# Optimization experiments

Measured on AMD Instinct MI355X. Metric: run time of the kernel, lower is better.

## Reference

```python
import jax, jax.numpy as jnp
import numpy as np

H, W, C_IN, C_OUT, B = 256, 256, 64, 64, 2
NEG_SLOPE = 0.2


def make_grid_edges(h, w, b):
    """8-neighborhood grid edges + self-loops (GATConv add_self_loops), batched with node offsets."""
    idx = np.arange(h * w).reshape(h, w)
    src_l, dst_l = [], []
    for dr in (-1, 0, 1):
        for dc in (-1, 0, 1):
            rs = slice(max(0, -dr), h - max(0, dr))
            cs = slice(max(0, -dc), w - max(0, dc))
            dst = idx[rs, cs]
            src = idx[rs.start + dr:rs.stop + dr, cs.start + dc:cs.stop + dc]
            src_l.append(src.ravel())
            dst_l.append(dst.ravel())
    s = np.concatenate(src_l)
    d = np.concatenate(dst_l)
    offs = (np.arange(b) * h * w)[:, None]
    return (s[None] + offs).ravel().astype(np.int32), (d[None] + offs).ravel().astype(np.int32)


def setup_inputs() -> dict:
    key = jax.random.key(0)
    ks = jax.random.split(key, 7)
    x = jax.random.normal(ks[0], (B, C_IN, H, W), dtype=jnp.float32)
    pos_w = jax.random.normal(ks[1], (2, C_IN), dtype=jnp.float32) * (1.0 / np.sqrt(2.0))
    pos_b = jax.random.normal(ks[2], (C_IN,), dtype=jnp.float32) * 0.1
    lin_w = jax.random.normal(ks[3], (C_IN, C_OUT), dtype=jnp.float32) * (1.0 / np.sqrt(C_IN))
    att_src = jax.random.normal(ks[4], (C_OUT,), dtype=jnp.float32) * (1.0 / np.sqrt(C_OUT))
    att_dst = jax.random.normal(ks[5], (C_OUT,), dtype=jnp.float32) * (1.0 / np.sqrt(C_OUT))
    bias = jax.random.normal(ks[6], (C_OUT,), dtype=jnp.float32) * 0.1
    es, ed = make_grid_edges(H, W, B)
    return {"x": x, "pos_w": pos_w, "pos_b": pos_b, "lin_w": lin_w,
            "att_src": att_src, "att_dst": att_dst, "bias": bias,
            "edge_src": jnp.asarray(es), "edge_dst": jnp.asarray(ed)}


def reference(x, pos_w, pos_b, lin_w, att_src, att_dst, bias, edge_src, edge_dst):
    b, c, h, w = x.shape
    n = h * w
    num_nodes = b * n
    # positional encoding: pos[h,w] = (y, x) in [-1,1]
    px = jnp.linspace(-1.0, 1.0, w)
    py = jnp.linspace(-1.0, 1.0, h)
    gx, gy = jnp.meshgrid(px, py, indexing="xy")          # (H, W)
    pos = jnp.stack([gy, gx], axis=-1)                     # (H, W, 2)
    pe = pos @ pos_w + pos_b                               # (H, W, C)
    xg = (x + pe.transpose(2, 0, 1)[None]).transpose(0, 2, 3, 1).reshape(num_nodes, c)
    # GATConv, heads=1: linear transform, per-edge attention logits
    hfeat = xg @ lin_w                                     # (BN, Cout)
    a_src = hfeat @ att_src                                # (BN,)
    a_dst = hfeat @ att_dst                                # (BN,)
    e = jax.nn.leaky_relu(a_src[edge_src] + a_dst[edge_dst], NEG_SLOPE)  # (E,)
    # segment softmax over incoming edges of each target node
    m = jax.ops.segment_max(e, edge_dst, num_segments=num_nodes)
    p = jnp.exp(e - m[edge_dst])
    s = jax.ops.segment_sum(p, edge_dst, num_segments=num_nodes)
    alpha = p / s[edge_dst]                                # (E,)
    # scatter-add aggregation of weighted messages
    out = jax.ops.segment_sum(alpha[:, None] * hfeat[edge_src], edge_dst,
                              num_segments=num_nodes) + bias
    return out.reshape(b, h, w, -1).transpose(0, 3, 1, 2)
```

## Files before the change

### kernel.cpp

```cpp
#include <hip/hip_runtime.h>

#define HGT 256
#define WID 256
#define CH  64
#define NB  2
#define HW  (HGT * WID)
#define NODES (NB * HW)
#define NEG_SLOPE 0.2f


__device__ __forceinline__ unsigned short f2bf(float f) {
    union { float f; unsigned u; } v; v.f = f;
    unsigned r = v.u + 0x7FFF + ((v.u >> 16) & 1);
    return (unsigned short)(r >> 16);
}

__global__ __launch_bounds__(256) void gat_feat(
    const float* __restrict__ x, const float* __restrict__ pos_w,
    const float* __restrict__ pos_b, const float* __restrict__ lin_w,
    const float* __restrict__ att_src, const float* __restrict__ att_dst,
    unsigned short* __restrict__ hfeat, float* __restrict__ asrc,
    float* __restrict__ adst)
{
    __shared__ float xs[CH][64];
    __shared__ float W0[CH], W1[CH], Bc[CH];
    __shared__ float red_s[4][64], red_d[4][64];

    const int tid = threadIdx.x;
    const int tx  = tid & 63;
    const int ty  = tid >> 6;

    const int raw = blockIdx.x;
    const int wg  = (raw & 7) * 256 + (raw >> 3);
    const int chunk = wg & 3;
    const int bi    = wg >> 2;
    const int i     = bi & (HGT - 1);
    const int b     = bi >> 8;
    const int j     = chunk * 64 + tx;
    const int hw    = i * WID + j;

    const float* xb = x + (size_t)b * CH * HW + hw;
    #pragma unroll
    for (int r = 0; r < 16; ++r) {
        const int ci = ty * 16 + r;
        xs[ci][tx] = xb[(size_t)ci * HW];
    }

    if (tid < CH) {
        float w0 = 0.f, w1 = 0.f, bc = 0.f;
        for (int ci = 0; ci < CH; ++ci) {
            float lwv = lin_w[ci * CH + tid];
            w0 = fmaf(pos_w[ci],      lwv, w0);
            w1 = fmaf(pos_w[CH + ci], lwv, w1);
            bc = fmaf(pos_b[ci],      lwv, bc);
        }
        W0[tid] = w0; W1[tid] = w1; Bc[tid] = bc;
    }
    __syncthreads();

    const int cob = __builtin_amdgcn_readfirstlane(ty) * 16;

    float acc[16];
    #pragma unroll
    for (int k = 0; k < 16; ++k) acc[k] = 0.f;

    const float* lw = lin_w + cob;
    #pragma unroll
    for (int ci = 0; ci < CH; ++ci) {
        const float xv = xs[ci][tx];
        #pragma unroll
        for (int k = 0; k < 16; ++k)
            acc[k] = fmaf(xv, lw[ci * CH + k], acc[k]);
    }

    const float py  = -1.f + (2.f / 255.f) * (float)i;
    const float pxv = -1.f + (2.f / 255.f) * (float)j;

    float as = 0.f, ad = 0.f;
    unsigned pk[8];
    #pragma unroll
    for (int k = 0; k < 16; ++k) {
        const int co = cob + k;
        const float h = acc[k] + py * W0[co] + pxv * W1[co] + Bc[co];
        as = fmaf(h, att_src[co], as);
        ad = fmaf(h, att_dst[co], ad);
        const unsigned short bf = f2bf(h);
        if (k & 1) pk[k >> 1] |= (unsigned)bf << 16;
        else       pk[k >> 1]  = bf;
    }
    uint2* hq = (uint2*)hfeat + (size_t)(b * 16 + (cob >> 2)) * HW + hw;
    #pragma unroll
    for (int qq = 0; qq < 4; ++qq)
        hq[(size_t)qq * HW] = make_uint2(pk[2 * qq], pk[2 * qq + 1]);

    red_s[ty][tx] = as; red_d[ty][tx] = ad;
    __syncthreads();
    if (ty == 0) {
        const int node = b * HW + hw;
        asrc[node] = red_s[0][tx] + red_s[1][tx] + red_s[2][tx] + red_s[3][tx];
        adst[node] = red_d[0][tx] + red_d[1][tx] + red_d[2][tx] + red_d[3][tx];
    }
}

__global__ __launch_bounds__(256) void gat_aggr(
    const unsigned short* __restrict__ hfeat, const float* __restrict__ asrc,
    const float* __restrict__ adst, const float* __restrict__ bias,
    float* __restrict__ out)
{
    const int tid = threadIdx.x;
    const int tx  = tid & 63;
    const int ty  = tid >> 6;

    const int raw = blockIdx.x;
    const int wg  = (raw & 7) * 1024 + (raw >> 3);
    const int qg    = wg & 3;
    const int chunk = (wg >> 2) & 3;
    const int bi    = wg >> 4;
    const int i     = bi & (HGT - 1);
    const int b     = bi >> 8;
    const int j     = chunk * 64 + tx;
    const int hw    = i * WID + j;
    const int node  = b * HW + hw;
    const int q     = __builtin_amdgcn_readfirstlane(qg * 4 + ty);

    const float adv = adst[node];

    float w[9];
    int   off[9];
    float m = -1e30f;
    #pragma unroll
    for (int t = 0; t < 9; ++t) {
        const int dr = t / 3 - 1, dc = t % 3 - 1;
        const int r = i + dr, c = j + dc;
        const bool ok = (r >= 0) && (r < HGT) && (c >= 0) && (c < WID);
        off[t] = ok ? (dr * WID + dc) : 0;
        float ev = -1e30f;
        if (ok) {
            ev = asrc[node + off[t]] + adv;
            ev = (ev >= 0.f) ? ev : NEG_SLOPE * ev;
        }
        w[t] = ev;
        m = fmaxf(m, ev);
    }

    float s = 0.f;
    #pragma unroll
    for (int t = 0; t < 9; ++t) {
        const float p = (w[t] > -1e29f) ? __expf(w[t] - m) : 0.f;
        w[t] = p; s += p;
    }
    const float inv = 1.f / s;

    const uint2* hq = (const uint2*)hfeat + (size_t)(b * 16 + q) * HW + hw;

    float a0 = 0.f, a1 = 0.f, a2 = 0.f, a3 = 0.f;
    #pragma unroll
    for (int t = 0; t < 9; ++t) {
        const uint2 v  = hq[off[t]];
        const float wt = w[t] * inv;
        a0 = fmaf(wt, __uint_as_float(v.x << 16),         a0);
        a1 = fmaf(wt, __uint_as_float(v.x & 0xffff0000u), a1);
        a2 = fmaf(wt, __uint_as_float(v.y << 16),         a2);
        a3 = fmaf(wt, __uint_as_float(v.y & 0xffff0000u), a3);
    }

    float* ob = out + (size_t)(b * CH + q * 4) * HW + hw;
    ob[0 * (size_t)HW] = a0 + bias[q * 4 + 0];
    ob[1 * (size_t)HW] = a1 + bias[q * 4 + 1];
    ob[2 * (size_t)HW] = a2 + bias[q * 4 + 2];
    ob[3 * (size_t)HW] = a3 + bias[q * 4 + 3];
}

extern "C" void kernel_launch(void* const* d_in, const int* in_sizes, int n_in,
                              void* d_out, int out_size, void* d_ws, size_t ws_size,
                              hipStream_t stream) {
    const float* x       = (const float*)d_in[0];
    const float* pos_w   = (const float*)d_in[1];
    const float* pos_b   = (const float*)d_in[2];
    const float* lin_w   = (const float*)d_in[3];
    const float* att_src = (const float*)d_in[4];
    const float* att_dst = (const float*)d_in[5];
    const float* bias    = (const float*)d_in[6];

    float* out = (float*)d_out;
    unsigned short* hfeat = (unsigned short*)d_ws;
    float* asrc = (float*)((char*)d_ws + (size_t)NODES * CH * 2);
    float* adst = asrc + NODES;

    gat_feat<<<dim3(2048), dim3(256), 0, stream>>>(
        x, pos_w, pos_b, lin_w, att_src, att_dst, hfeat, asrc, adst);
    gat_aggr<<<dim3(8192), dim3(256), 0, stream>>>(
        hfeat, asrc, adst, bias, out);
}
```

Before: 150.2 us.

## Compute node feature projection with bf16 MFMA instead of scalar FMA

Rewrites the feature-projection kernel so each wavefront handles 32 nodes and runs the 64x64 linear transform as bf16 32x32x16 MFMA instructions. The lin_w weights are converted to bf16 and stored swizzled in LDS, and x is cast to bf16 in registers. This replaces the scalar FMA loop and its LDS staging of x. It also changes the launch to 512 blocks of 512 threads and reduces the attention dot products with a lane shuffle. The cost is lower precision, since both the inputs and the weights are now rounded to bf16 before the matmul.

```diff
diff --git a/kernel.cpp b/kernel.cpp
--- a/kernel.cpp
+++ b/kernel.cpp
@@ -8,6 +8,8 @@
 #define NODES (NB * HW)
 #define NEG_SLOPE 0.2f
 
+typedef float f32x16 __attribute__((ext_vector_type(16)));
+typedef short short8 __attribute__((ext_vector_type(8)));
 
 __device__ __forceinline__ unsigned short f2bf(float f) {
     union { float f; unsigned u; } v; v.f = f;
@@ -15,91 +17,127 @@
     return (unsigned short)(r >> 16);
 }
 
-__global__ __launch_bounds__(256) void gat_feat(
+__global__ __launch_bounds__(512) void gat_feat(
     const float* __restrict__ x, const float* __restrict__ pos_w,
     const float* __restrict__ pos_b, const float* __restrict__ lin_w,
     const float* __restrict__ att_src, const float* __restrict__ att_dst,
     unsigned short* __restrict__ hfeat, float* __restrict__ asrc,
     float* __restrict__ adst)
 {
-    __shared__ float xs[CH][64];
-    __shared__ float W0[CH], W1[CH], Bc[CH];
-    __shared__ float red_s[4][64], red_d[4][64];
-
-    const int tid = threadIdx.x;
-    const int tx  = tid & 63;
-    const int ty  = tid >> 6;
-
-    const int raw = blockIdx.x;
-    const int wg  = (raw & 7) * 256 + (raw >> 3);
-    const int chunk = wg & 3;
-    const int bi    = wg >> 2;
-    const int i     = bi & (HGT - 1);
-    const int b     = bi >> 8;
-    const int j     = chunk * 64 + tx;
-    const int hw    = i * WID + j;
-
-    const float* xb = x + (size_t)b * CH * HW + hw;
-    #pragma unroll
-    for (int r = 0; r < 16; ++r) {
-        const int ci = ty * 16 + r;
-        xs[ci][tx] = xb[(size_t)ci * HW];
-    }
-
+    __shared__ __align__(16) unsigned char wlds[CH * 128];
+    __shared__ __align__(16) float W0s[CH], W1s[CH], Bcs[CH], atts[CH], attd[CH];
+
+    const int tid  = threadIdx.x;
+    const int lane = tid & 63;
+    const int wid  = tid >> 6;
+    const int hi   = lane >> 5;
+    const int col  = lane & 31;
+
+    {
+        const int co  = tid & 63;
+        const int cib = (tid >> 6) * 8;
+        unsigned char* rowp = wlds + co * 128;
+        const unsigned sw = (unsigned)((co & 7) << 4);
+        #pragma unroll
+        for (int p = 0; p < 4; ++p) {
+            const int ci = cib + 2 * p;
+            const unsigned lo = f2bf(lin_w[ci * CH + co]);
+            const unsigned hh = f2bf(lin_w[(ci + 1) * CH + co]);
+            *(unsigned*)(rowp + (((unsigned)(2 * ci)) ^ sw)) = lo | (hh << 16);
+        }
+    }
     if (tid < CH) {
         float w0 = 0.f, w1 = 0.f, bc = 0.f;
         for (int ci = 0; ci < CH; ++ci) {
-            float lwv = lin_w[ci * CH + tid];
+            const float lwv = lin_w[ci * CH + tid];
             w0 = fmaf(pos_w[ci],      lwv, w0);
             w1 = fmaf(pos_w[CH + ci], lwv, w1);
             bc = fmaf(pos_b[ci],      lwv, bc);
         }
-        W0[tid] = w0; W1[tid] = w1; Bc[tid] = bc;
+        W0s[tid] = w0; W1s[tid] = w1; Bcs[tid] = bc;
+    } else if (tid < 128) {
+        atts[tid - 64] = att_src[tid - 64];
+    } else if (tid < 192) {
+        attd[tid - 128] = att_dst[tid - 128];
     }
     __syncthreads();
 
-    const int cob = __builtin_amdgcn_readfirstlane(ty) * 16;
-
-    float acc[16];
-    #pragma unroll
-    for (int k = 0; k < 16; ++k) acc[k] = 0.f;
-
-    const float* lw = lin_w + cob;
-    #pragma unroll
-    for (int ci = 0; ci < CH; ++ci) {
-        const float xv = xs[ci][tx];
-        #pragma unroll
-        for (int k = 0; k < 16; ++k)
-            acc[k] = fmaf(xv, lw[ci * CH + k], acc[k]);
-    }
-
-    const float py  = -1.f + (2.f / 255.f) * (float)i;
-    const float pxv = -1.f + (2.f / 255.f) * (float)j;
-
+    short8 a0[4], a1[4];
+    {
+        const unsigned sw = (unsigned)((col & 7) << 4);
+        #pragma unroll
+        for (int ks = 0; ks < 4; ++ks) {
+            const unsigned off = (unsigned)(32 * ks + 16 * hi) ^ sw;
+            a0[ks] = *(const short8*)(wlds + col * 128 + off);
+            a1[ks] = *(const short8*)(wlds + (32 + col) * 128 + off);
+        }
+    }
+
+    const int g     = blockIdx.x * 8 + wid;
+    const int node0 = g * 32;
+    const int b     = node0 >> 16;
+    const int hw    = (node0 & (HW - 1)) + col;
+    const int node  = node0 + col;
+
+    const float* xp = x + (size_t)b * CH * HW + hw;
+    float xv[32];
+    #pragma unroll
+    for (int ks = 0; ks < 4; ++ks)
+        #pragma unroll
+        for (int e = 0; e < 8; ++e)
+            xv[ks * 8 + e] = xp[(size_t)(16 * ks + 8 * hi + e) * HW];
+
+    short8 bk[4];
+    #pragma unroll
+    for (int ks = 0; ks < 4; ++ks)
+        #pragma unroll
+        for (int e = 0; e < 8; ++e)
+            bk[ks][e] = (short)f2bf(xv[ks * 8 + e]);
+
+    f32x16 acc0, acc1;
+    #pragma unroll
+    for (int k = 0; k < 16; ++k) { acc0[k] = 0.f; acc1[k] = 0.f; }
+
+    #pragma unroll
+    for (int ks = 0; ks < 4; ++ks) {
+        acc0 = __builtin_amdgcn_mfma_f32_32x32x16_bf16(a0[ks], bk[ks], acc0, 0, 0, 0);
+        acc1 = __builtin_amdgcn_mfma_f32_32x32x16_bf16(a1[ks], bk[ks], acc1, 0, 0, 0);
+    }
+
+    const int ii = hw >> 8, jj = hw & 255;
+    const float py = -1.f + (2.f / 255.f) * (float)ii;
+    const float px = -1.f + (2.f / 255.f) * (float)jj;
+
+    uint2* hq = (uint2*)hfeat + (size_t)b * 16 * HW + hw;
     float as = 0.f, ad = 0.f;
-    unsigned pk[8];
-    #pragma unroll
-    for (int k = 0; k < 16; ++k) {
-        const int co = cob + k;
-        const float h = acc[k] + py * W0[co] + pxv * W1[co] + Bc[co];
-        as = fmaf(h, att_src[co], as);
-        ad = fmaf(h, att_dst[co], ad);
-        const unsigned short bf = f2bf(h);
-        if (k & 1) pk[k >> 1] |= (unsigned)bf << 16;
-        else       pk[k >> 1]  = bf;
-    }
-    uint2* hq = (uint2*)hfeat + (size_t)(b * 16 + (cob >> 2)) * HW + hw;
-    #pragma unroll
-    for (int qq = 0; qq < 4; ++qq)
-        hq[(size_t)qq * HW] = make_uint2(pk[2 * qq], pk[2 * qq + 1]);
-
-    red_s[ty][tx] = as; red_d[ty][tx] = ad;
-    __syncthreads();
-    if (ty == 0) {
-        const int node = b * HW + hw;
-        asrc[node] = red_s[0][tx] + red_s[1][tx] + red_s[2][tx] + red_s[3][tx];
-        adst[node] = red_d[0][tx] + red_d[1][tx] + red_d[2][tx] + red_d[3][tx];
-    }
+
+    #pragma unroll
+    for (int t = 0; t < 2; ++t) {
+        const f32x16 A = (t == 0) ? acc0 : acc1;
+        #pragma unroll
+        for (int q2 = 0; q2 < 4; ++q2) {
+            const int cb = 32 * t + 8 * q2 + 4 * hi;
+            const float4 w0 = *(const float4*)&W0s[cb];
+            const float4 w1 = *(const float4*)&W1s[cb];
+            const float4 bc = *(const float4*)&Bcs[cb];
+            const float4 s4 = *(const float4*)&atts[cb];
+            const float4 d4 = *(const float4*)&attd[cb];
+            const float h0 = A[4 * q2 + 0] + py * w0.x + px * w1.x + bc.x;
+            const float h1 = A[4 * q2 + 1] + py * w0.y + px * w1.y + bc.y;
+            const float h2 = A[4 * q2 + 2] + py * w0.z + px * w1.z + bc.z;
+            const float h3 = A[4 * q2 + 3] + py * w0.w + px * w1.w + bc.w;
+            as += h0 * s4.x + h1 * s4.y + h2 * s4.z + h3 * s4.w;
+            ad += h0 * d4.x + h1 * d4.y + h2 * d4.z + h3 * d4.w;
+            const unsigned u0 = (unsigned)f2bf(h0) | ((unsigned)f2bf(h1) << 16);
+            const unsigned u1 = (unsigned)f2bf(h2) | ((unsigned)f2bf(h3) << 16);
+            const int q = 8 * t + 2 * q2 + hi;
+            hq[(size_t)q * HW] = make_uint2(u0, u1);
+        }
+    }
+
+    as += __shfl_xor(as, 32);
+    ad += __shfl_xor(ad, 32);
+    if (hi == 0) { asrc[node] = as; adst[node] = ad; }
 }
 
 __global__ __launch_bounds__(256) void gat_aggr(
@@ -187,7 +225,7 @@
     float* asrc = (float*)((char*)d_ws + (size_t)NODES * CH * 2);
     float* adst = asrc + NODES;
 
-    gat_feat<<<dim3(2048), dim3(256), 0, stream>>>(
+    gat_feat<<<dim3(512), dim3(512), 0, stream>>>(
         x, pos_w, pos_b, lin_w, att_src, att_dst, hfeat, asrc, adst);
     gat_aggr<<<dim3(8192), dim3(256), 0, stream>>>(
         hfeat, asrc, adst, bias, out);
```

After: 125.9 us. 16.2% less time.
